# Optimization experiments

Hardware: AMD Instinct MI355X
Metric: run time of the kernel (lower is better)

## Reference

```python
import jax, jax.numpy as jnp
import numpy as np
import math

EPS = 1e-12  # F.normalize default eps

def _l2_normalize(x):
    n = jnp.sqrt(jnp.sum(x * x, axis=-1, keepdims=True))
    return x / jnp.maximum(n, EPS)

def setup_inputs() -> dict:
    key = jax.random.key(0)
    k1, k2 = jax.random.split(key)
    B, F, C = 16384, 1024, 1000
    features = jax.random.normal(k1, (B, F), dtype=jnp.float32)
    prototypes = jax.random.normal(k2, (C, F), dtype=jnp.float32)
    distance_scale = jnp.ones((1,), dtype=jnp.float32)
    temperature = jnp.ones((1,), dtype=jnp.float32)
    return {"features": features, "prototypes": prototypes,
            "distance_scale": distance_scale, "temperature": temperature}

def reference(features, prototypes, distance_scale, temperature):
    # L2-normalize both sides (F.normalize, p=2, eps=1e-12)
    f = _l2_normalize(features)      # [B, F]
    p = _l2_normalize(prototypes)    # [C, F]
    # Pairwise Euclidean distance. For unit vectors ||f-p||^2 = 2 - 2 f.p,
    # clamped at 0 for numerical safety; then / sqrt(2).
    sim = jnp.einsum('bf,cf->bc', f, p)                  # [B, C]
    sq = jnp.maximum(2.0 - 2.0 * sim, 0.0)
    distances = jnp.sqrt(sq) / jnp.float32(math.sqrt(2.0))
    iso = jnp.abs(distance_scale) * distances            # [B, C]
    logits = -(iso + jnp.mean(iso, axis=1, keepdims=True))
    return logits / temperature
```

## Files before the change

kernel.cpp:

```cpp
#include <hip/hip_runtime.h>
#include <hip/hip_bf16.h>
#include <math.h>

#define B_ROWS 16384
#define C_COLS 1000
#define C_PAD  1024
#define FDIM   1024
#define FBLKS  4096
#define FP8_SCALE 256.0f
#define INV_SIM   (1.0f / (FP8_SCALE * FP8_SCALE))

typedef __attribute__((ext_vector_type(8))) short bf16x8;
typedef __attribute__((ext_vector_type(4))) float f32x4;
typedef __attribute__((ext_vector_type(4))) int   i32x4;
typedef __attribute__((ext_vector_type(8))) int   i32x8;

#define GLD_LDS(gp, lp) __builtin_amdgcn_global_load_lds( \
    (__attribute__((address_space(1))) void*)(gp),        \
    (__attribute__((address_space(3))) void*)(lp), 16, 0, 0)

__global__ __launch_bounds__(256) void normalize_all(
    const float* __restrict__ feat, const float* __restrict__ prot,
    unsigned char* __restrict__ fb, unsigned char* __restrict__ pb,
    float* __restrict__ rowsum)
{
    const int lane = threadIdx.x & 63;
    const int wave = threadIdx.x >> 6;

    if (blockIdx.x < 64) rowsum[blockIdx.x * 256 + threadIdx.x] = 0.0f;

    const float* in;
    unsigned char* out;
    int row, nvalid;
    if (blockIdx.x < FBLKS) {
        row = blockIdx.x * 4 + wave;  in = feat; out = fb; nvalid = B_ROWS;
    } else {
        row = (blockIdx.x - FBLKS) * 4 + wave;  in = prot; out = pb; nvalid = C_COLS;
    }
    unsigned char* orow = out + (size_t)row * FDIM;

    if (row >= nvalid) {
        i32x4 z = {0, 0, 0, 0};
        ((i32x4*)orow)[lane] = z;
        return;
    }

    const float4* rp = (const float4*)(in + (size_t)row * FDIM);
    float4 v[4];
    float ss = 0.0f;
    #pragma unroll
    for (int c = 0; c < 4; ++c) {
        v[c] = rp[lane * 4 + c];
        ss += v[c].x * v[c].x + v[c].y * v[c].y + v[c].z * v[c].z + v[c].w * v[c].w;
    }
    #pragma unroll
    for (int off = 1; off < 64; off <<= 1) ss += __shfl_xor(ss, off, 64);
    const float inv = FP8_SCALE / sqrtf(fmaxf(ss, 1e-24f));

    i32x4 pk;
    #pragma unroll
    for (int c = 0; c < 4; ++c) {
        int w0 = __builtin_amdgcn_cvt_pk_fp8_f32(v[c].x * inv, v[c].y * inv, 0, false);
        w0     = __builtin_amdgcn_cvt_pk_fp8_f32(v[c].z * inv, v[c].w * inv, w0, true);
        pk[c] = w0;
    }
    ((i32x4*)orow)[lane] = pk;
}

__global__ __launch_bounds__(512, 2) void gemm_dist(
    const unsigned char* __restrict__ A,
    const unsigned char* __restrict__ Bp,
    __hip_bfloat16* __restrict__ D,
    float* __restrict__ rowsum)
{
    extern __shared__ unsigned char LDS[];
    unsigned char* As = LDS;
    unsigned char* Bs = LDS + 65536;

    const int tid  = threadIdx.x;
    const int lane = tid & 63;
    const int wave = tid >> 6;

    const int id  = blockIdx.x;
    const int xcd = id & 7;
    const int seq = id >> 3;
    const int bn  = seq & 3;
    const int bm  = xcd * 8 + (seq >> 2);

    const int waveM = (wave >> 2) * 128;
    const int waveN = (wave & 3) * 64;

    f32x4 acc[8][4] = {};

    const int srow8 = lane >> 3;
    const int sg    = (lane & 7) ^ srow8;
    const unsigned char* Abase = A  + ((size_t)(bm * 256 + wave * 32 + srow8)) * FDIM + sg * 16;
    const unsigned char* Bbase = Bp + ((size_t)(bn * 256 + wave * 32 + srow8)) * FDIM + sg * 16;
    const int ldsW = wave * 4096;

    const int q2   = (lane >> 4) * 2;
    const int bxor = lane & 7;
    const int fA = (waveM + (lane & 15)) * 128;
    const int fB = (waveN + (lane & 15)) * 128;
    const int pg0 = ((q2)     ^ bxor) * 16;
    const int pg1 = ((q2 + 1) ^ bxor) * 16;

#define STAGE_BATCH(K0_, BUF_) do {                                                  \
        _Pragma("unroll")                                                            \
        for (int r_ = 0; r_ < 4; ++r_)                                               \
            GLD_LDS(Abase + (size_t)(r_ * 8) * FDIM + (K0_), &As[(BUF_) + ldsW + r_ * 1024]); \
        _Pragma("unroll")                                                            \
        for (int r_ = 0; r_ < 4; ++r_)                                               \
            GLD_LDS(Bbase + (size_t)(r_ * 8) * FDIM + (K0_), &Bs[(BUF_) + ldsW + r_ * 1024]); \
    } while (0)

#define COMPUTE_STEP(CUR_) do {                                                      \
        i32x8 b4[4], a4[4];                                                          \
        _Pragma("unroll")                                                            \
        for (int nt = 0; nt < 4; ++nt) {                                             \
            ((i32x4*)&b4[nt])[0] = *(const i32x4*)&Bs[(CUR_) + fB + nt * 2048 + pg0];\
            ((i32x4*)&b4[nt])[1] = *(const i32x4*)&Bs[(CUR_) + fB + nt * 2048 + pg1];\
        }                                                                            \
        _Pragma("unroll")                                                            \
        for (int mt = 0; mt < 4; ++mt) {                                             \
            ((i32x4*)&a4[mt])[0] = *(const i32x4*)&As[(CUR_) + fA + mt * 2048 + pg0];\
            ((i32x4*)&a4[mt])[1] = *(const i32x4*)&As[(CUR_) + fA + mt * 2048 + pg1];\
        }                                                                            \
        __builtin_amdgcn_s_setprio(1);                                               \
        _Pragma("unroll")                                                            \
        for (int mt = 0; mt < 4; ++mt)                                               \
            _Pragma("unroll")                                                        \
            for (int nt = 0; nt < 4; ++nt)                                           \
                acc[mt][nt] = __builtin_amdgcn_mfma_scale_f32_16x16x128_f8f6f4(      \
                    a4[mt], b4[nt], acc[mt][nt], 0, 0, 0, 127, 0, 127);              \
        __builtin_amdgcn_s_setprio(0);                                               \
        _Pragma("unroll")                                                            \
        for (int mt = 0; mt < 4; ++mt) {                                             \
            ((i32x4*)&a4[mt])[0] = *(const i32x4*)&As[(CUR_) + fA + (mt + 4) * 2048 + pg0]; \
            ((i32x4*)&a4[mt])[1] = *(const i32x4*)&As[(CUR_) + fA + (mt + 4) * 2048 + pg1]; \
        }                                                                            \
        __builtin_amdgcn_s_setprio(1);                                               \
        _Pragma("unroll")                                                            \
        for (int mt = 0; mt < 4; ++mt)                                               \
            _Pragma("unroll")                                                        \
            for (int nt = 0; nt < 4; ++nt)                                           \
                acc[mt + 4][nt] = __builtin_amdgcn_mfma_scale_f32_16x16x128_f8f6f4(  \
                    a4[mt], b4[nt], acc[mt + 4][nt], 0, 0, 0, 127, 0, 127);          \
        __builtin_amdgcn_s_setprio(0);                                               \
    } while (0)

    STAGE_BATCH(0, 0);
    __builtin_amdgcn_sched_barrier(0);
    STAGE_BATCH(128, 32768);
    __builtin_amdgcn_sched_barrier(0);

    #pragma unroll 1
    for (int t = 0; t < 7; ++t) {
        asm volatile("s_waitcnt vmcnt(8)" ::: "memory");
        __builtin_amdgcn_s_barrier();
        __builtin_amdgcn_sched_barrier(0);

        const int cur = (t & 1) << 15;

        COMPUTE_STEP(cur);

        asm volatile("s_waitcnt lgkmcnt(0)" ::: "memory");
        __builtin_amdgcn_s_barrier();
        __builtin_amdgcn_sched_barrier(0);
        if (t < 6) {
            const int k0n = (t + 2) * 128;
            STAGE_BATCH(k0n, cur);
            __builtin_amdgcn_sched_barrier(0);
        }
    }

    asm volatile("s_waitcnt vmcnt(0)" ::: "memory");
    __builtin_amdgcn_s_barrier();
    __builtin_amdgcn_sched_barrier(0);
    COMPUTE_STEP(32768);

    const int row0 = bm * 256 + waveM;
    const int col0 = bn * 256 + waveN;
    #pragma unroll
    for (int mt = 0; mt < 8; ++mt) {
        #pragma unroll
        for (int r = 0; r < 4; ++r) {
            const int row = row0 + mt * 16 + (lane >> 4) * 4 + r;
            float part = 0.0f;
            #pragma unroll
            for (int nt = 0; nt < 4; ++nt) {
                const int col = col0 + nt * 16 + (lane & 15);
                const float sim = acc[mt][nt][r] * INV_SIM;
                const float dv = sqrtf(fmaxf(1.0f - sim, 0.0f));
                if (col < C_COLS) {
                    D[(size_t)row * C_COLS + col] = __float2bfloat16(dv);
                    part += dv;
                }
            }
            part += __shfl_xor(part, 1, 64);
            part += __shfl_xor(part, 2, 64);
            part += __shfl_xor(part, 4, 64);
            part += __shfl_xor(part, 8, 64);
            if ((lane & 15) == 0) atomicAdd(&rowsum[row], part);
        }
    }
}

__global__ __launch_bounds__(256) void finalize(
    const __hip_bfloat16* __restrict__ D, const float* __restrict__ rowsum,
    const float* __restrict__ scale, const float* __restrict__ temp,
    float* __restrict__ out)
{
    const size_t i = (size_t)blockIdx.x * 256 + threadIdx.x;
    const float a = -fabsf(scale[0]) / temp[0];
    const int row = (int)((i * 8) / C_COLS);
    const float m = rowsum[row] * (1.0f / (float)C_COLS);

    const bf16x8 dv = *(const bf16x8*)(D + i * 8);
    const __hip_bfloat16* dp = (const __hip_bfloat16*)&dv;
    float4 o0, o1;
    o0.x = a * (__bfloat162float(dp[0]) + m);
    o0.y = a * (__bfloat162float(dp[1]) + m);
    o0.z = a * (__bfloat162float(dp[2]) + m);
    o0.w = a * (__bfloat162float(dp[3]) + m);
    o1.x = a * (__bfloat162float(dp[4]) + m);
    o1.y = a * (__bfloat162float(dp[5]) + m);
    o1.z = a * (__bfloat162float(dp[6]) + m);
    o1.w = a * (__bfloat162float(dp[7]) + m);
    ((float4*)out)[i * 2]     = o0;
    ((float4*)out)[i * 2 + 1] = o1;
}

extern "C" void kernel_launch(void* const* d_in, const int* in_sizes, int n_in,
                              void* d_out, int out_size, void* d_ws, size_t ws_size,
                              hipStream_t stream)
{
    const float* features = (const float*)d_in[0];
    const float* protos   = (const float*)d_in[1];
    const float* dscale   = (const float*)d_in[2];
    const float* temp     = (const float*)d_in[3];
    float* out = (float*)d_out;

    char* ws = (char*)d_ws;
    unsigned char* fb = (unsigned char*)ws;
    unsigned char* pb = (unsigned char*)(ws + 16777216);
    __hip_bfloat16* D = (__hip_bfloat16*)(ws + 17825792);
    float* rowsum     = (float*)(ws + 50593792);

    static int lds_ok = 0;
    if (!lds_ok) {
        (void)hipFuncSetAttribute(reinterpret_cast<const void*>(gemm_dist),
                                  hipFuncAttributeMaxDynamicSharedMemorySize, 131072);
        lds_ok = 1;
    }

    normalize_all<<<FBLKS + C_PAD / 4, 256, 0, stream>>>(features, protos, fb, pb, rowsum);

    gemm_dist<<<256, 512, 131072, stream>>>(fb, pb, D, rowsum);

    finalize<<<(B_ROWS * C_COLS / 8) / 256, 256, 0, stream>>>(D, rowsum, dscale, temp, out);
}
```

Measured before the change: 159.9 us.

## Split K-step compute into four barrier-synchronised phases and fold tail into loop

Each K-step now runs in four phases. Each phase loads two A fragments (plus the B fragments in the first phase) and issues eight MFMAs, with workgroup barriers around each phase so the waves stay in lockstep. The final compute step moves into the main loop by widening it to eight iterations with a conditional vmcnt wait. The goal is to interleave LDS reads with MFMA work and keep waves aligned for better matrix-core overlap. In exchange it adds several barriers per K-step, which could stall waves.

Measured after the change: 162.2 us. No clear change (+1.4%).

```diff
diff --git a/kernel.cpp b/kernel.cpp
--- a/kernel.cpp
+++ b/kernel.cpp
@@ -114,70 +114,58 @@
             GLD_LDS(Bbase + (size_t)(r_ * 8) * FDIM + (K0_), &Bs[(BUF_) + ldsW + r_ * 1024]); \
     } while (0)
 
-#define COMPUTE_STEP(CUR_) do {                                                      \
-        i32x8 b4[4], a4[4];                                                          \
-        _Pragma("unroll")                                                            \
-        for (int nt = 0; nt < 4; ++nt) {                                             \
-            ((i32x4*)&b4[nt])[0] = *(const i32x4*)&Bs[(CUR_) + fB + nt * 2048 + pg0];\
-            ((i32x4*)&b4[nt])[1] = *(const i32x4*)&Bs[(CUR_) + fB + nt * 2048 + pg1];\
-        }                                                                            \
-        _Pragma("unroll")                                                            \
-        for (int mt = 0; mt < 4; ++mt) {                                             \
-            ((i32x4*)&a4[mt])[0] = *(const i32x4*)&As[(CUR_) + fA + mt * 2048 + pg0];\
-            ((i32x4*)&a4[mt])[1] = *(const i32x4*)&As[(CUR_) + fA + mt * 2048 + pg1];\
-        }                                                                            \
-        __builtin_amdgcn_s_setprio(1);                                               \
-        _Pragma("unroll")                                                            \
-        for (int mt = 0; mt < 4; ++mt)                                               \
-            _Pragma("unroll")                                                        \
-            for (int nt = 0; nt < 4; ++nt)                                           \
-                acc[mt][nt] = __builtin_amdgcn_mfma_scale_f32_16x16x128_f8f6f4(      \
-                    a4[mt], b4[nt], acc[mt][nt], 0, 0, 0, 127, 0, 127);              \
-        __builtin_amdgcn_s_setprio(0);                                               \
-        _Pragma("unroll")                                                            \
-        for (int mt = 0; mt < 4; ++mt) {                                             \
-            ((i32x4*)&a4[mt])[0] = *(const i32x4*)&As[(CUR_) + fA + (mt + 4) * 2048 + pg0]; \
-            ((i32x4*)&a4[mt])[1] = *(const i32x4*)&As[(CUR_) + fA + (mt + 4) * 2048 + pg1]; \
-        }                                                                            \
-        __builtin_amdgcn_s_setprio(1);                                               \
-        _Pragma("unroll")                                                            \
-        for (int mt = 0; mt < 4; ++mt)                                               \
-            _Pragma("unroll")                                                        \
-            for (int nt = 0; nt < 4; ++nt)                                           \
-                acc[mt + 4][nt] = __builtin_amdgcn_mfma_scale_f32_16x16x128_f8f6f4(  \
-                    a4[mt], b4[nt], acc[mt + 4][nt], 0, 0, 0, 127, 0, 127);          \
-        __builtin_amdgcn_s_setprio(0);                                               \
-    } while (0)
-
     STAGE_BATCH(0, 0);
     __builtin_amdgcn_sched_barrier(0);
     STAGE_BATCH(128, 32768);
     __builtin_amdgcn_sched_barrier(0);
 
     #pragma unroll 1
-    for (int t = 0; t < 7; ++t) {
-        asm volatile("s_waitcnt vmcnt(8)" ::: "memory");
+    for (int t = 0; t < 8; ++t) {
+        const int cur = (t & 1) << 15;
+
+        if (t < 7) { asm volatile("s_waitcnt vmcnt(8)" ::: "memory"); }
+        else       { asm volatile("s_waitcnt vmcnt(0)" ::: "memory"); }
         __builtin_amdgcn_s_barrier();
         __builtin_amdgcn_sched_barrier(0);
 
-        const int cur = (t & 1) << 15;
-
-        COMPUTE_STEP(cur);
-
-        asm volatile("s_waitcnt lgkmcnt(0)" ::: "memory");
-        __builtin_amdgcn_s_barrier();
-        __builtin_amdgcn_sched_barrier(0);
-        if (t < 6) {
-            const int k0n = (t + 2) * 128;
-            STAGE_BATCH(k0n, cur);
+        i32x8 b4[4];
+        #pragma unroll
+        for (int p = 0; p < 4; ++p) {
+            if (p == 0) {
+                #pragma unroll
+                for (int nt = 0; nt < 4; ++nt) {
+                    ((i32x4*)&b4[nt])[0] = *(const i32x4*)&Bs[cur + fB + nt * 2048 + pg0];
+                    ((i32x4*)&b4[nt])[1] = *(const i32x4*)&Bs[cur + fB + nt * 2048 + pg1];
+                }
+            }
+            i32x8 a2[2];
+            #pragma unroll
+            for (int m2 = 0; m2 < 2; ++m2) {
+                const int mt = p * 2 + m2;
+                ((i32x4*)&a2[m2])[0] = *(const i32x4*)&As[cur + fA + mt * 2048 + pg0];
+                ((i32x4*)&a2[m2])[1] = *(const i32x4*)&As[cur + fA + mt * 2048 + pg1];
+            }
+            if (p == 0) { asm volatile("s_waitcnt lgkmcnt(8)" ::: "memory"); }
+            __builtin_amdgcn_s_barrier();
+            asm volatile("s_waitcnt lgkmcnt(0)" ::: "memory");
+            __builtin_amdgcn_sched_barrier(0);
+            __builtin_amdgcn_s_setprio(1);
+            #pragma unroll
+            for (int m2 = 0; m2 < 2; ++m2)
+                #pragma unroll
+                for (int nt = 0; nt < 4; ++nt)
+                    acc[p * 2 + m2][nt] = __builtin_amdgcn_mfma_scale_f32_16x16x128_f8f6f4(
+                        a2[m2], b4[nt], acc[p * 2 + m2][nt], 0, 0, 0, 127, 0, 127);
+            __builtin_amdgcn_s_setprio(0);
+            __builtin_amdgcn_s_barrier();
             __builtin_amdgcn_sched_barrier(0);
         }
-    }
-
-    asm volatile("s_waitcnt vmcnt(0)" ::: "memory");
-    __builtin_amdgcn_s_barrier();
-    __builtin_amdgcn_sched_barrier(0);
-    COMPUTE_STEP(32768);
+
+        if (t < 6) {
+            STAGE_BATCH((t + 2) * 128, cur);
+            __builtin_amdgcn_sched_barrier(0);
+        }
+    }
 
     const int row0 = bm * 256 + waveM;
     const int col0 = bn * 256 + waveN;
```
